# Kernel optimization log

Hardware: AMD Instinct MI355X
Metric: run time of the kernel (lower is better)

The kernel has to match this reference:

```python
import jax, jax.numpy as jnp
import numpy as np

SPATIAL_SHAPES = ((100, 100), (50, 50), (25, 25), (13, 13))
B, C, NH, NL, NP, DFF = 4, 256, 8, 4, 4, 1024
HD = C // NH
L = sum(h * w for h, w in SPATIAL_SHAPES)  # 13294


def _xavier(key, shape):
    s = (6.0 / (shape[0] + shape[1])) ** 0.5
    return jax.random.uniform(key, shape, jnp.float32, -s, s)


def setup_inputs():
    key = jax.random.key(0)
    ks = jax.random.split(key, 12)
    ss = jnp.array(SPATIAL_SHAPES, jnp.int32)
    lsi = jnp.concatenate([jnp.zeros((1,), jnp.int32), jnp.cumsum(ss[:, 0] * ss[:, 1])[:-1].astype(jnp.int32)])
    return {
        "query": jax.random.normal(ks[0], (B, L, C), jnp.float32),
        "query_pos": jax.random.normal(ks[1], (B, L, C), jnp.float32),
        "reference_points": jax.random.uniform(ks[2], (B, L, NL, 2), jnp.float32),
        "spatial_shapes": ss,
        "level_start_index": lsi,
        "v_W": _xavier(ks[3], (C, C)), "v_b": jnp.zeros((C,), jnp.float32),
        "off_W": 0.01 * jax.random.normal(ks[4], (C, NH * NL * NP * 2), jnp.float32),
        "off_b": 0.1 * jax.random.normal(ks[5], (NH * NL * NP * 2,), jnp.float32),
        "aw_W": 0.01 * jax.random.normal(ks[6], (C, NH * NL * NP), jnp.float32),
        "aw_b": jnp.zeros((NH * NL * NP,), jnp.float32),
        "out_W": _xavier(ks[7], (C, C)), "out_b": jnp.zeros((C,), jnp.float32),
        "ln1_g": jnp.ones((C,), jnp.float32), "ln1_b": jnp.zeros((C,), jnp.float32),
        "lin1_W": _xavier(ks[8], (C, DFF)), "lin1_b": jnp.zeros((DFF,), jnp.float32),
        "lin2_W": _xavier(ks[9], (DFF, C)), "lin2_b": jnp.zeros((C,), jnp.float32),
        "ln2_g": jnp.ones((C,), jnp.float32), "ln2_b": jnp.zeros((C,), jnp.float32),
    }


def _layer_norm(x, g, b):
    mu = x.mean(-1, keepdims=True)
    var = ((x - mu) ** 2).mean(-1, keepdims=True)
    return (x - mu) * jax.lax.rsqrt(var + 1e-5) * g + b


def _msda(q, value, reference_points, v_W, v_b, off_W, off_b, aw_W, aw_b, out_W, out_b):
    # value projection, split heads -> [B, NH, L, HD]
    v = (value @ v_W + v_b).reshape(B, L, NH, HD).transpose(0, 2, 1, 3)
    off = (q @ off_W + off_b).reshape(B, L, NH, NL, NP, 2)
    aw = jax.nn.softmax((q @ aw_W + aw_b).reshape(B, L, NH, NL * NP), axis=-1)
    aw = aw.reshape(B, L, NH, NL, NP).transpose(0, 2, 1, 3, 4)  # [B,NH,L,NL,NP]
    # offset normalizer is (W, H) per level, matching (x, y) coords
    norm = jnp.array([[w, h] for h, w in SPATIAL_SHAPES], q.dtype)
    loc = reference_points[:, :, None, :, None, :] + off / norm[None, None, None, :, None, :]
    loc = loc.transpose(0, 2, 1, 3, 4, 5)  # [B,NH,L,NL,NP,2]
    acc = jnp.zeros((B, NH, L, HD), q.dtype)
    start = 0
    for l, (H_, W_) in enumerate(SPATIAL_SHAPES):
        v_l = jax.lax.dynamic_slice_in_dim(v, start, H_ * W_, axis=2)  # [B,NH,HW,HD]
        # grid_sample(align_corners=False): pixel = loc*size - 0.5
        x = loc[:, :, :, l, :, 0] * W_ - 0.5  # [B,NH,L,NP]
        y = loc[:, :, :, l, :, 1] * H_ - 0.5
        x0 = jnp.floor(x); y0 = jnp.floor(y)
        lx = x - x0; ly = y - y0
        x0i = x0.astype(jnp.int32); y0i = y0.astype(jnp.int32)

        def corner(yi, xi, w):
            valid = (yi >= 0) & (yi < H_) & (xi >= 0) & (xi < W_)  # zero padding
            idx = jnp.clip(yi, 0, H_ - 1) * W_ + jnp.clip(xi, 0, W_ - 1)
            g = jnp.take_along_axis(v_l, idx.reshape(B, NH, L * NP, 1), axis=2)
            g = g.reshape(B, NH, L, NP, HD)
            return g * (w * valid)[..., None]

        s = (corner(y0i, x0i, (1 - ly) * (1 - lx))
             + corner(y0i, x0i + 1, (1 - ly) * lx)
             + corner(y0i + 1, x0i, ly * (1 - lx))
             + corner(y0i + 1, x0i + 1, ly * lx))  # [B,NH,L,NP,HD]
        acc = acc + (s * aw[:, :, :, l, :, None]).sum(3)
        start += H_ * W_
    out = acc.transpose(0, 2, 1, 3).reshape(B, L, C)
    return out @ out_W + out_b


def _forward(query, query_pos, reference_points, v_W, v_b, off_W, off_b, aw_W, aw_b,
             out_W, out_b, ln1_g, ln1_b, lin1_W, lin1_b, lin2_W, lin2_b, ln2_g, ln2_b):
    q = query + query_pos
    src2 = _msda(q, query, reference_points, v_W, v_b, off_W, off_b, aw_W, aw_b, out_W, out_b)
    x = _layer_norm(query + src2, ln1_g, ln1_b)
    ffn = jax.nn.relu(x @ lin1_W + lin1_b) @ lin2_W + lin2_b
    return _layer_norm(x + ffn, ln2_g, ln2_b)


def reference(query, query_pos, reference_points, spatial_shapes, level_start_index,
              v_W, v_b, off_W, off_b, aw_W, aw_b, out_W, out_b,
              ln1_g, ln1_b, lin1_W, lin1_b, lin2_W, lin2_b, ln2_g, ln2_b):
    # spatial_shapes / level_start_index are consistent with the static SPATIAL_SHAPES
    # constant (shapes must be static for reshapes under jit).
    return _forward(query, query_pos, reference_points, v_W, v_b, off_W, off_b, aw_W, aw_b,
                    out_W, out_b, ln1_g, ln1_b, lin1_W, lin1_b, lin2_W, lin2_b, ln2_g, ln2_b)
```

## Files before the change

### kernel.cpp

```cpp
#include <hip/hip_runtime.h>
#include <hip/hip_bf16.h>
#include <cstddef>

constexpr int Ll   = 13294;
constexpr int NROW = 4 * Ll;
constexpr int MP   = 53248;

typedef __bf16       bf8v __attribute__((ext_vector_type(8)));
typedef __bf16       bf2v __attribute__((ext_vector_type(2)));
typedef float        f4v  __attribute__((ext_vector_type(4)));
typedef unsigned int u4v  __attribute__((ext_vector_type(4)));

#if defined(__has_builtin)
#  if __has_builtin(__builtin_amdgcn_fdot2_f32_bf16)
#    define HAVE_DOT2_BF16 1
#  endif
#endif
#ifndef HAVE_DOT2_BF16
#  define HAVE_DOT2_BF16 0
#endif

__device__ __forceinline__ void xcd_remap(int& m0, int& n0)
{
    const int nwg  = gridDim.x * gridDim.y;
    const int flat = blockIdx.y * gridDim.x + blockIdx.x;
    const int w    = (flat & 7) * (nwg >> 3) + (flat >> 3);
    n0 = (w % gridDim.x) * 128;
    m0 = (w / gridDim.x) * 128;
}

template<bool RELU, bool OUTF, bool OUTB>
__global__ __launch_bounds__(256)
void gemm_mfma(const __hip_bfloat16* __restrict__ A, const __hip_bfloat16* __restrict__ Bt,
               const float* __restrict__ bias, const float* __restrict__ bias2,
               float* __restrict__ Cf, __hip_bfloat16* __restrict__ Cb,
               int M, int N, int K)
{
    __shared__ __hip_bfloat16 As[128 * 32];
    __shared__ __hip_bfloat16 Bs[128 * 32];
    const int tid  = threadIdx.x;
    const int wid  = tid >> 6;
    const int lane = tid & 63;
    int m0, n0;
    xcd_remap(m0, n0);
    const int wm = wid >> 1, wn = wid & 1;
    const int fr = lane & 15, fq = lane >> 4;
    const int sr = lane >> 2;
    const int sc = (lane & 3) * 8;

    f4v acc[4][4] = {};

    for (int k0 = 0; k0 < K; k0 += 32) {
        #pragma unroll
        for (int i = 0; i < 2; ++i) {
            const int s = wid * 2 + i;
            const __hip_bfloat16* sa = A  + (size_t)(m0 + s * 16 + sr) * K + k0 + sc;
            const __hip_bfloat16* sb = Bt + (size_t)(n0 + s * 16 + sr) * K + k0 + sc;
            __builtin_amdgcn_global_load_lds(
                (const __attribute__((address_space(1))) void*)sa,
                (__attribute__((address_space(3))) void*)&As[s * 512], 16, 0, 0);
            __builtin_amdgcn_global_load_lds(
                (const __attribute__((address_space(1))) void*)sb,
                (__attribute__((address_space(3))) void*)&Bs[s * 512], 16, 0, 0);
        }
        __syncthreads();

        bf8v a[4], b[4];
        #pragma unroll
        for (int r = 0; r < 4; ++r) {
            a[r] = __builtin_bit_cast(bf8v, *(const u4v*)&As[(wm * 64 + r * 16 + fr) * 32 + fq * 8]);
            b[r] = __builtin_bit_cast(bf8v, *(const u4v*)&Bs[(wn * 64 + r * 16 + fr) * 32 + fq * 8]);
        }
        #pragma unroll
        for (int nr = 0; nr < 4; ++nr)
            #pragma unroll
            for (int mr = 0; mr < 4; ++mr)
                acc[nr][mr] = __builtin_amdgcn_mfma_f32_16x16x32_bf16(b[nr], a[mr], acc[nr][mr], 0, 0, 0);
        __syncthreads();
    }

    #pragma unroll
    for (int nr = 0; nr < 4; ++nr) {
        const int colbase = n0 + wn * 64 + nr * 16 + fq * 4;
        const float* bp = (bias2 != nullptr && colbase >= 256) ? (bias2 - 256) : bias;
        const float4 b4 = *(const float4*)&bp[colbase];
        #pragma unroll
        for (int mr = 0; mr < 4; ++mr) {
            const int row = m0 + wm * 64 + mr * 16 + fr;
            f4v v = acc[nr][mr];
            v[0] += b4.x; v[1] += b4.y; v[2] += b4.z; v[3] += b4.w;
            if (RELU) {
                v[0] = fmaxf(v[0], 0.f); v[1] = fmaxf(v[1], 0.f);
                v[2] = fmaxf(v[2], 0.f); v[3] = fmaxf(v[3], 0.f);
            }
            if (OUTF)
                *(float4*)&Cf[(size_t)row * N + colbase] = make_float4(v[0], v[1], v[2], v[3]);
            if (OUTB) {
                union { ushort4 u; __hip_bfloat16 h[4]; } pk;
                pk.h[0] = __float2bfloat16(v[0]); pk.h[1] = __float2bfloat16(v[1]);
                pk.h[2] = __float2bfloat16(v[2]); pk.h[3] = __float2bfloat16(v[3]);
                *(ushort4*)&Cb[(size_t)row * N + colbase] = pk.u;
            }
        }
    }
}

template<bool STOREB, bool RESB>
__global__ __launch_bounds__(256)
void gemm_ln(const __hip_bfloat16* __restrict__ A, const __hip_bfloat16* __restrict__ Bt,
             const float* __restrict__ bias,
             const float* __restrict__ resF, const __hip_bfloat16* __restrict__ resB,
             int Mres,
             const float* __restrict__ g, const float* __restrict__ be,
             float* __restrict__ outF, int MstoreF,
             __hip_bfloat16* __restrict__ outB,
             int K)
{
    __shared__ __hip_bfloat16 As[64 * 32];
    __shared__ __hip_bfloat16 Bs[256 * 32];
    __shared__ float red[2][64][2];
    const int tid  = threadIdx.x;
    const int wid  = tid >> 6;
    const int lane = tid & 63;
    const int m0 = blockIdx.x * 64;
    const int wm = wid >> 1, wn = wid & 1;
    const int fr = lane & 15, fq = lane >> 4;
    const int sr = lane >> 2;
    const int sc = (lane & 3) * 8;

    f4v acc[8][2] = {};

    for (int k0 = 0; k0 < K; k0 += 32) {
        {
            const __hip_bfloat16* sa = A + (size_t)(m0 + wid * 16 + sr) * K + k0 + sc;
            __builtin_amdgcn_global_load_lds(
                (const __attribute__((address_space(1))) void*)sa,
                (__attribute__((address_space(3))) void*)&As[wid * 512], 16, 0, 0);
        }
        #pragma unroll
        for (int i = 0; i < 4; ++i) {
            const int s = wid * 4 + i;
            const __hip_bfloat16* sb = Bt + (size_t)(s * 16 + sr) * K + k0 + sc;
            __builtin_amdgcn_global_load_lds(
                (const __attribute__((address_space(1))) void*)sb,
                (__attribute__((address_space(3))) void*)&Bs[s * 512], 16, 0, 0);
        }
        __syncthreads();

        bf8v a[2], b[8];
        #pragma unroll
        for (int r = 0; r < 2; ++r)
            a[r] = __builtin_bit_cast(bf8v, *(const u4v*)&As[(wm * 32 + r * 16 + fr) * 32 + fq * 8]);
        #pragma unroll
        for (int r = 0; r < 8; ++r)
            b[r] = __builtin_bit_cast(bf8v, *(const u4v*)&Bs[(wn * 128 + r * 16 + fr) * 32 + fq * 8]);
        #pragma unroll
        for (int nr = 0; nr < 8; ++nr)
            #pragma unroll
            for (int mr = 0; mr < 2; ++mr)
                acc[nr][mr] = __builtin_amdgcn_mfma_f32_16x16x32_bf16(b[nr], a[mr], acc[nr][mr], 0, 0, 0);
        __syncthreads();
    }

    float s2[2] = {}, q2[2] = {};
    #pragma unroll
    for (int nr = 0; nr < 8; ++nr) {
        const int colbase = wn * 128 + nr * 16 + fq * 4;
        const float4 b4 = *(const float4*)&bias[colbase];
        #pragma unroll
        for (int mr = 0; mr < 2; ++mr) {
            const int row = m0 + wm * 32 + mr * 16 + fr;
            f4v x = acc[nr][mr];
            x[0] += b4.x; x[1] += b4.y; x[2] += b4.z; x[3] += b4.w;
            if (RESB) {
                const ushort4 r4 = *(const ushort4*)&resB[(size_t)row * 256 + colbase];
                x[0] += __builtin_bit_cast(float, (unsigned)r4.x << 16);
                x[1] += __builtin_bit_cast(float, (unsigned)r4.y << 16);
                x[2] += __builtin_bit_cast(float, (unsigned)r4.z << 16);
                x[3] += __builtin_bit_cast(float, (unsigned)r4.w << 16);
            } else if (row < Mres) {
                const float4 r4 = *(const float4*)&resF[(size_t)row * 256 + colbase];
                x[0] += r4.x; x[1] += r4.y; x[2] += r4.z; x[3] += r4.w;
            }
            acc[nr][mr] = x;
            s2[mr] += x[0] + x[1] + x[2] + x[3];
            q2[mr] += x[0]*x[0] + x[1]*x[1] + x[2]*x[2] + x[3]*x[3];
        }
    }
    #pragma unroll
    for (int mr = 0; mr < 2; ++mr) {
        s2[mr] += __shfl_xor(s2[mr], 16, 64);
        q2[mr] += __shfl_xor(q2[mr], 16, 64);
        s2[mr] += __shfl_xor(s2[mr], 32, 64);
        q2[mr] += __shfl_xor(q2[mr], 32, 64);
    }
    if (fq == 0) {
        #pragma unroll
        for (int mr = 0; mr < 2; ++mr) {
            red[wn][wm * 32 + mr * 16 + fr][0] = s2[mr];
            red[wn][wm * 32 + mr * 16 + fr][1] = q2[mr];
        }
    }
    __syncthreads();
    float mean[2], rinv[2];
    #pragma unroll
    for (int mr = 0; mr < 2; ++mr) {
        const int r = wm * 32 + mr * 16 + fr;
        const float ss = red[0][r][0] + red[1][r][0];
        const float qq = red[0][r][1] + red[1][r][1];
        mean[mr] = ss * (1.f / 256.f);
        const float var = qq * (1.f / 256.f) - mean[mr] * mean[mr];
        rinv[mr] = rsqrtf(var + 1e-5f);
    }
    #pragma unroll
    for (int nr = 0; nr < 8; ++nr) {
        const int colbase = wn * 128 + nr * 16 + fq * 4;
        const float4 g4 = *(const float4*)&g[colbase];
        const float4 e4 = *(const float4*)&be[colbase];
        #pragma unroll
        for (int mr = 0; mr < 2; ++mr) {
            const int row = m0 + wm * 32 + mr * 16 + fr;
            const f4v x = acc[nr][mr];
            float y0 = (x[0] - mean[mr]) * rinv[mr] * g4.x + e4.x;
            float y1 = (x[1] - mean[mr]) * rinv[mr] * g4.y + e4.y;
            float y2 = (x[2] - mean[mr]) * rinv[mr] * g4.z + e4.z;
            float y3 = (x[3] - mean[mr]) * rinv[mr] * g4.w + e4.w;
            if (row < MstoreF)
                *(float4*)&outF[(size_t)row * 256 + colbase] = make_float4(y0, y1, y2, y3);
            if (STOREB) {
                union { ushort4 u; __hip_bfloat16 h[4]; } pk;
                pk.h[0] = __float2bfloat16(y0); pk.h[1] = __float2bfloat16(y1);
                pk.h[2] = __float2bfloat16(y2); pk.h[3] = __float2bfloat16(y3);
                *(ushort4*)&outB[(size_t)row * 256 + colbase] = pk.u;
            }
        }
    }
}

__global__ __launch_bounds__(256)
void prep_weights(const float* __restrict__ vW, const float* __restrict__ offW,
                  const float* __restrict__ awW, const float* __restrict__ outW,
                  const float* __restrict__ w1, const float* __restrict__ w2,
                  __hip_bfloat16* __restrict__ vWt, __hip_bfloat16* __restrict__ catWt,
                  __hip_bfloat16* __restrict__ outWt, __hip_bfloat16* __restrict__ w1t,
                  __hip_bfloat16* __restrict__ w2t)
{
    int i = blockIdx.x * 256 + threadIdx.x;
    if (i < 65536) { const int n = i >> 8, k = i & 255;
        vWt[i] = __float2bfloat16(vW[(size_t)k * 256 + n]); return; }
    i -= 65536;
    if (i < 98304) { const int n = i >> 8, k = i & 255;
        catWt[i] = __float2bfloat16(n < 256 ? offW[(size_t)k * 256 + n]
                                            : awW[(size_t)k * 128 + n - 256]); return; }
    i -= 98304;
    if (i < 65536) { const int n = i >> 8, k = i & 255;
        outWt[i] = __float2bfloat16(outW[(size_t)k * 256 + n]); return; }
    i -= 65536;
    if (i < 262144) { const int n = i >> 8, k = i & 255;
        w1t[i] = __float2bfloat16(w1[(size_t)k * 1024 + n]); return; }
    i -= 262144;
    { const int n = i >> 10, k = i & 1023;
        w2t[i] = __float2bfloat16(w2[(size_t)k * 256 + n]); }
}

__global__ __launch_bounds__(256)
void cvt_both(const float* __restrict__ q, const float* __restrict__ qp,
              __hip_bfloat16* __restrict__ qb, __hip_bfloat16* __restrict__ qpb)
{
    const int i   = blockIdx.x * 256 + threadIdx.x;
    const int row = i >> 5;
    union { u4v u; __hip_bfloat16 h[8]; } p1, p2;
    if (row >= NROW) {
        u4v z = {0u, 0u, 0u, 0u};
        p1.u = z; p2.u = z;
    } else {
        const size_t e = (size_t)i * 8;
        float4 x0 = *(const float4*)&q[e];
        float4 x1 = *(const float4*)&q[e + 4];
        float4 y0 = *(const float4*)&qp[e];
        float4 y1 = *(const float4*)&qp[e + 4];
        p1.h[0] = __float2bfloat16(x0.x); p1.h[1] = __float2bfloat16(x0.y);
        p1.h[2] = __float2bfloat16(x0.z); p1.h[3] = __float2bfloat16(x0.w);
        p1.h[4] = __float2bfloat16(x1.x); p1.h[5] = __float2bfloat16(x1.y);
        p1.h[6] = __float2bfloat16(x1.z); p1.h[7] = __float2bfloat16(x1.w);
        p2.h[0] = __float2bfloat16(x0.x + y0.x); p2.h[1] = __float2bfloat16(x0.y + y0.y);
        p2.h[2] = __float2bfloat16(x0.z + y0.z); p2.h[3] = __float2bfloat16(x0.w + y0.w);
        p2.h[4] = __float2bfloat16(x1.x + y1.x); p2.h[5] = __float2bfloat16(x1.y + y1.y);
        p2.h[6] = __float2bfloat16(x1.z + y1.z); p2.h[7] = __float2bfloat16(x1.w + y1.w);
    }
    *(u4v*)&qb[(size_t)i * 8]  = p1.u;
    *(u4v*)&qpb[(size_t)i * 8] = p2.u;
}

__device__ __forceinline__ float blo(unsigned u) { return __builtin_bit_cast(float, u << 16); }
__device__ __forceinline__ float bhi(unsigned u) { return __builtin_bit_cast(float, u & 0xffff0000u); }

__global__ __launch_bounds__(256)
void msda_sample4(const __hip_bfloat16* __restrict__ v, const float* __restrict__ cat,
                  const float* __restrict__ refp, __hip_bfloat16* __restrict__ accO)
{
    __shared__ int      sIdx[1024][4];
    __shared__ unsigned sWpk[1024][2];
    const int row0 = blockIdx.x * 8;
    const int tid  = threadIdx.x;

    #pragma unroll
    for (int it = 0; it < 4; ++it) {
        const int item = it * 256 + tid;
        const int p = item & 15, h = (item >> 4) & 7, r = item >> 7;
        const int row = row0 + r;
        const int lvl = p >> 2;
        const float logit = cat[(size_t)row * 384 + 256 + h * 16 + p];
        float mx = logit;
        #pragma unroll
        for (int o = 1; o < 16; o <<= 1) mx = fmaxf(mx, __shfl_xor(mx, o, 64));
        const float e = __expf(logit - mx);
        float s = e;
        #pragma unroll
        for (int o = 1; o < 16; o <<= 1) s += __shfl_xor(s, o, 64);
        const float aw = e / s;

        const int Hs_[4] = {100, 50, 25, 13};
        const int Ss[4]  = {0, 10000, 12500, 13125};
        const int   Wl = Hs_[lvl];
        const float Wf = (float)Wl;
        const float ox = cat[(size_t)row * 384 + h * 32 + p * 2 + 0];
        const float oy = cat[(size_t)row * 384 + h * 32 + p * 2 + 1];
        const float rx = refp[(size_t)row * 8 + lvl * 2 + 0];
        const float ry = refp[(size_t)row * 8 + lvl * 2 + 1];
        const float x = (rx + ox / Wf) * Wf - 0.5f;
        const float y = (ry + oy / Wf) * Wf - 0.5f;
        const float x0f = floorf(x), y0f = floorf(y);
        const float lx = x - x0f, ly = y - y0f;
        const int x0 = (int)x0f, y0 = (int)y0f;
        const int b = row / Ll;
        const int vbase = b * Ll + Ss[lvl];
        int ixr[4]; unsigned short wb[4];
        #pragma unroll
        for (int c = 0; c < 4; ++c) {
            const int cy = c >> 1, cx = c & 1;
            const int yi = y0 + cy, xi = x0 + cx;
            const bool ok = (yi >= 0) & (yi < Wl) & (xi >= 0) & (xi < Wl);
            const int yc = min(max(yi, 0), Wl - 1);
            const int xc = min(max(xi, 0), Wl - 1);
            const float wt = (cy ? ly : 1.f - ly) * (cx ? lx : 1.f - lx);
            ixr[c] = (vbase + yc * Wl + xc) * 512;
            const __hip_bfloat16 hw = __float2bfloat16(ok ? aw * wt : 0.f);
            wb[c] = __builtin_bit_cast(unsigned short, hw);
        }
        const int item2 = (item & ~15) | ((item & 15) ^ h);
        *(int4*)&sIdx[item2][0] = make_int4(ixr[0], ixr[1], ixr[2], ixr[3]);
        sWpk[item2][0] = (unsigned)wb[0] | ((unsigned)wb[1] << 16);
        sWpk[item2][1] = (unsigned)wb[2] | ((unsigned)wb[3] << 16);
    }
    __syncthreads();

    const int r   = tid >> 5;
    const int h   = (tid >> 2) & 7;
    const int oct = tid & 3;
    const int row = row0 + r;
    const char* vB = (const char*)v + (h * 32 + oct * 8) * 2;
    const int ibase = r * 128 + h * 16;
    float acc[8] = {};
    #pragma unroll
    for (int i = 0; i < 16; ++i) {
        const int idx = ibase + (i ^ h);
        const int4  ix = *(const int4*)&sIdx[idx][0];
        const uint2 wp = *(const uint2*)&sWpk[idx][0];
        u4v u0 = *(const u4v*)(vB + (unsigned)ix.x);
        u4v u1 = *(const u4v*)(vB + (unsigned)ix.y);
        u4v u2 = *(const u4v*)(vB + (unsigned)ix.z);
        u4v u3 = *(const u4v*)(vB + (unsigned)ix.w);
#if HAVE_DOT2_BF16
        const bf2v w01 = __builtin_bit_cast(bf2v, wp.x);
        const bf2v w23 = __builtin_bit_cast(bf2v, wp.y);
        #pragma unroll
        for (int q = 0; q < 4; ++q) {
            const unsigned lo01 = __builtin_amdgcn_perm(u1[q], u0[q], 0x05040100u);
            const unsigned hi01 = __builtin_amdgcn_perm(u1[q], u0[q], 0x07060302u);
            const unsigned lo23 = __builtin_amdgcn_perm(u3[q], u2[q], 0x05040100u);
            const unsigned hi23 = __builtin_amdgcn_perm(u3[q], u2[q], 0x07060302u);
            acc[2*q]   = __builtin_amdgcn_fdot2_f32_bf16(__builtin_bit_cast(bf2v, lo01), w01, acc[2*q],   false);
            acc[2*q]   = __builtin_amdgcn_fdot2_f32_bf16(__builtin_bit_cast(bf2v, lo23), w23, acc[2*q],   false);
            acc[2*q+1] = __builtin_amdgcn_fdot2_f32_bf16(__builtin_bit_cast(bf2v, hi01), w01, acc[2*q+1], false);
            acc[2*q+1] = __builtin_amdgcn_fdot2_f32_bf16(__builtin_bit_cast(bf2v, hi23), w23, acc[2*q+1], false);
        }
#else
        const float w0 = blo(wp.x), w1 = bhi(wp.x);
        const float w2 = blo(wp.y), w3 = bhi(wp.y);
        #pragma unroll
        for (int q = 0; q < 4; ++q) {
            acc[2*q]   = fmaf(w0, blo(u0[q]), acc[2*q]);
            acc[2*q+1] = fmaf(w0, bhi(u0[q]), acc[2*q+1]);
            acc[2*q]   = fmaf(w1, blo(u1[q]), acc[2*q]);
            acc[2*q+1] = fmaf(w1, bhi(u1[q]), acc[2*q+1]);
            acc[2*q]   = fmaf(w2, blo(u2[q]), acc[2*q]);
            acc[2*q+1] = fmaf(w2, bhi(u2[q]), acc[2*q+1]);
            acc[2*q]   = fmaf(w3, blo(u3[q]), acc[2*q]);
            acc[2*q+1] = fmaf(w3, bhi(u3[q]), acc[2*q+1]);
        }
#endif
    }
    union { u4v u; __hip_bfloat16 hh[8]; } pk;
    #pragma unroll
    for (int q = 0; q < 8; ++q) pk.hh[q] = __float2bfloat16(acc[q]);
    *(u4v*)&accO[(size_t)row * 256 + h * 32 + oct * 8] = pk.u;
}

extern "C" void kernel_launch(void* const* d_in, const int* in_sizes, int n_in,
                              void* d_out, int out_size, void* d_ws, size_t ws_size,
                              hipStream_t stream)
{
    (void)in_sizes; (void)n_in; (void)out_size; (void)ws_size;
    const float* query = (const float*)d_in[0];
    const float* qpos  = (const float*)d_in[1];
    const float* refp  = (const float*)d_in[2];
    const float* v_W   = (const float*)d_in[5];
    const float* v_b   = (const float*)d_in[6];
    const float* off_W = (const float*)d_in[7];
    const float* off_b = (const float*)d_in[8];
    const float* aw_W  = (const float*)d_in[9];
    const float* aw_b  = (const float*)d_in[10];
    const float* out_W = (const float*)d_in[11];
    const float* out_b = (const float*)d_in[12];
    const float* ln1g  = (const float*)d_in[13];
    const float* ln1b  = (const float*)d_in[14];
    const float* w1    = (const float*)d_in[15];
    const float* b1    = (const float*)d_in[16];
    const float* w2    = (const float*)d_in[17];
    const float* b2    = (const float*)d_in[18];
    const float* ln2g  = (const float*)d_in[19];
    const float* ln2b  = (const float*)d_in[20];
    float* out = (float*)d_out;

    char* ws = (char*)d_ws;
    constexpr size_t CATF_B = (size_t)MP * 384 * 4;
    constexpr size_t HALF_B = (size_t)MP * 256 * 2;
    float*          catf = (float*)ws;
    __hip_bfloat16* qb   = (__hip_bfloat16*)(ws + CATF_B);
    __hip_bfloat16* qpb  = (__hip_bfloat16*)(ws + CATF_B + HALF_B);
    __hip_bfloat16* vbuf = (__hip_bfloat16*)(ws + CATF_B + 2 * HALF_B);
    __hip_bfloat16* accb = qb;
    __hip_bfloat16* xb   = vbuf;
    __hip_bfloat16* hbuf = (__hip_bfloat16*)ws;
    char* wsw = ws + CATF_B + 3 * HALF_B;
    __hip_bfloat16* vWt   = (__hip_bfloat16*)(wsw);
    __hip_bfloat16* catWt = (__hip_bfloat16*)(wsw + 131072);
    __hip_bfloat16* outWt = (__hip_bfloat16*)(wsw + 327680);
    __hip_bfloat16* w1t   = (__hip_bfloat16*)(wsw + 458752);
    __hip_bfloat16* w2t   = (__hip_bfloat16*)(wsw + 983040);

    dim3 blk(256);

    prep_weights<<<2944, blk, 0, stream>>>(v_W, off_W, aw_W, out_W, w1, w2,
                                           vWt, catWt, outWt, w1t, w2t);
    cvt_both<<<MP / 8, blk, 0, stream>>>(query, qpos, qb, qpb);

    gemm_mfma<false, false, true><<<dim3(2, MP / 128), blk, 0, stream>>>(
        qb, vWt, v_b, nullptr, nullptr, vbuf, MP, 256, 256);
    gemm_mfma<false, true, false><<<dim3(3, MP / 128), blk, 0, stream>>>(
        qpb, catWt, off_b, aw_b, catf, nullptr, MP, 384, 256);

    msda_sample4<<<NROW / 8, blk, 0, stream>>>(vbuf, catf, refp, accb);

    gemm_ln<true, false><<<MP / 64, blk, 0, stream>>>(
        accb, outWt, out_b, query, nullptr, NROW, ln1g, ln1b,
        nullptr, 0, xb, 256);

    gemm_mfma<true, false, true><<<dim3(8, MP / 128), blk, 0, stream>>>(
        xb, w1t, b1, nullptr, nullptr, hbuf, MP, 1024, 256);

    gemm_ln<false, true><<<MP / 64, blk, 0, stream>>>(
        hbuf, w2t, b2, nullptr, xb, MP, ln2g, ln2b,
        out, NROW, nullptr, 1024);
}
```

Measured before the change: 357.6 us.

## Store offset/logit projection in bf16, remap sampler blocks per XCD, use bf16 residual

The offset/attention-logit GEMM now writes bf16 instead of fp32, halving that intermediate's write and read traffic in the sampler. The sampler gains an XCD-aware block remap so neighbouring rows land on the same XCD for L2 locality. The first LayerNorm GEMM reads the residual from the bf16 copy of the query instead of fp32. The workspace layout is reshuffled to match. Offsets and logits lose precision, which can move sampling positions slightly.

```diff
diff --git a/kernel.cpp b/kernel.cpp
--- a/kernel.cpp
+++ b/kernel.cpp
@@ -296,12 +296,21 @@
 __device__ __forceinline__ float bhi(unsigned u) { return __builtin_bit_cast(float, u & 0xffff0000u); }
 
 __global__ __launch_bounds__(256)
-void msda_sample4(const __hip_bfloat16* __restrict__ v, const float* __restrict__ cat,
+void msda_sample5(const __hip_bfloat16* __restrict__ v, const __hip_bfloat16* __restrict__ cat,
                   const float* __restrict__ refp, __hip_bfloat16* __restrict__ accO)
 {
     __shared__ int      sIdx[1024][4];
     __shared__ unsigned sWpk[1024][2];
-    const int row0 = blockIdx.x * 8;
+    int blk;
+    {
+        const int nwg  = gridDim.x;
+        const int q    = nwg >> 3;
+        const int r    = nwg & 7;
+        const int xcd  = blockIdx.x & 7;
+        const int off  = blockIdx.x >> 3;
+        blk = (xcd < r ? xcd * (q + 1) : r * (q + 1) + (xcd - r) * q) + off;
+    }
+    const int row0 = blk * 8;
     const int tid  = threadIdx.x;
 
     #pragma unroll
@@ -310,7 +319,7 @@
         const int p = item & 15, h = (item >> 4) & 7, r = item >> 7;
         const int row = row0 + r;
         const int lvl = p >> 2;
-        const float logit = cat[(size_t)row * 384 + 256 + h * 16 + p];
+        const float logit = __bfloat162float(cat[(size_t)row * 384 + 256 + h * 16 + p]);
         float mx = logit;
         #pragma unroll
         for (int o = 1; o < 16; o <<= 1) mx = fmaxf(mx, __shfl_xor(mx, o, 64));
@@ -324,8 +333,8 @@
         const int Ss[4]  = {0, 10000, 12500, 13125};
         const int   Wl = Hs_[lvl];
         const float Wf = (float)Wl;
-        const float ox = cat[(size_t)row * 384 + h * 32 + p * 2 + 0];
-        const float oy = cat[(size_t)row * 384 + h * 32 + p * 2 + 1];
+        const float ox = __bfloat162float(cat[(size_t)row * 384 + h * 32 + p * 2 + 0]);
+        const float oy = __bfloat162float(cat[(size_t)row * 384 + h * 32 + p * 2 + 1]);
         const float rx = refp[(size_t)row * 8 + lvl * 2 + 0];
         const float ry = refp[(size_t)row * 8 + lvl * 2 + 1];
         const float x = (rx + ox / Wf) * Wf - 0.5f;
@@ -434,16 +443,17 @@
     float* out = (float*)d_out;
 
     char* ws = (char*)d_ws;
-    constexpr size_t CATF_B = (size_t)MP * 384 * 4;
     constexpr size_t HALF_B = (size_t)MP * 256 * 2;
-    float*          catf = (float*)ws;
-    __hip_bfloat16* qb   = (__hip_bfloat16*)(ws + CATF_B);
-    __hip_bfloat16* qpb  = (__hip_bfloat16*)(ws + CATF_B + HALF_B);
-    __hip_bfloat16* vbuf = (__hip_bfloat16*)(ws + CATF_B + 2 * HALF_B);
-    __hip_bfloat16* accb = qb;
+    constexpr size_t CATB_B = (size_t)MP * 384 * 2;
+    constexpr size_t HBUF_B = (size_t)MP * 1024 * 2;
+    __hip_bfloat16* hbuf = (__hip_bfloat16*)ws;
+    __hip_bfloat16* qb   = (__hip_bfloat16*)ws;
+    __hip_bfloat16* qpb  = (__hip_bfloat16*)(ws + HALF_B);
+    __hip_bfloat16* catb = (__hip_bfloat16*)(ws + 2 * HALF_B);
+    __hip_bfloat16* vbuf = (__hip_bfloat16*)(ws + HBUF_B);
+    __hip_bfloat16* accb = qpb;
     __hip_bfloat16* xb   = vbuf;
-    __hip_bfloat16* hbuf = (__hip_bfloat16*)ws;
-    char* wsw = ws + CATF_B + 3 * HALF_B;
+    char* wsw = ws + HBUF_B + HALF_B;
     __hip_bfloat16* vWt   = (__hip_bfloat16*)(wsw);
     __hip_bfloat16* catWt = (__hip_bfloat16*)(wsw + 131072);
     __hip_bfloat16* outWt = (__hip_bfloat16*)(wsw + 327680);
@@ -458,13 +468,13 @@
 
     gemm_mfma<false, false, true><<<dim3(2, MP / 128), blk, 0, stream>>>(
         qb, vWt, v_b, nullptr, nullptr, vbuf, MP, 256, 256);
-    gemm_mfma<false, true, false><<<dim3(3, MP / 128), blk, 0, stream>>>(
-        qpb, catWt, off_b, aw_b, catf, nullptr, MP, 384, 256);
-
-    msda_sample4<<<NROW / 8, blk, 0, stream>>>(vbuf, catf, refp, accb);
-
-    gemm_ln<true, false><<<MP / 64, blk, 0, stream>>>(
-        accb, outWt, out_b, query, nullptr, NROW, ln1g, ln1b,
+    gemm_mfma<false, false, true><<<dim3(3, MP / 128), blk, 0, stream>>>(
+        qpb, catWt, off_b, aw_b, nullptr, catb, MP, 384, 256);
+
+    msda_sample5<<<NROW / 8, blk, 0, stream>>>(vbuf, catb, refp, accb);
+
+    gemm_ln<true, true><<<MP / 64, blk, 0, stream>>>(
+        accb, outWt, out_b, nullptr, qb, MP, ln1g, ln1b,
         nullptr, 0, xb, 256);
 
     gemm_mfma<true, false, true><<<dim3(8, MP / 128), blk, 0, stream>>>(
```

Result: faster. 348.2 us (-2.6%).
